# Kernel optimization log

Measured on AMD Instinct MI355X. Metric: run time of the kernel, lower is better.

The kernel has to match this reference:

```python
import jax, jax.numpy as jnp
import numpy as np

E = 300000
N_ATOMS = 10000
C = 256
RBF = 16
NUM_TARGET = 1


def setup_inputs() -> dict:
    key = jax.random.key(0)
    ks = jax.random.split(key, 12)
    s = lambda fan_in: 1.0 / np.sqrt(fan_in)
    return {
        "x": jax.random.normal(ks[0], (E, C), dtype=jnp.float32),
        "rbf": jax.random.uniform(ks[1], (E, RBF), dtype=jnp.float32),
        "num_atoms": N_ATOMS,
        "edge_index_0": jax.random.randint(ks[2], (E,), 0, N_ATOMS, dtype=jnp.int64),
        # lin_rbf: Linear(rbf_dim -> in_channels)
        "w_rbf": jax.random.normal(ks[3], (C, RBF), dtype=jnp.float32) * s(RBF),
        "b_rbf": jnp.zeros((C,), dtype=jnp.float32),
        # mlp: Linear(C,C), SiLU, Linear(C,C), SiLU, Linear(C, num_target)
        "w1": jax.random.normal(ks[4], (C, C), dtype=jnp.float32) * s(C),
        "b1": jnp.zeros((C,), dtype=jnp.float32),
        "w2": jax.random.normal(ks[5], (C, C), dtype=jnp.float32) * s(C),
        "b2": jnp.zeros((C,), dtype=jnp.float32),
        "w3": jax.random.normal(ks[6], (NUM_TARGET, C), dtype=jnp.float32) * s(C),
        "b3": jnp.zeros((NUM_TARGET,), dtype=jnp.float32),
    }


def reference(x, rbf, num_atoms, edge_index_0, w_rbf, b_rbf, w1, b1, w2, b2, w3, b3):
    # rbf_filter = lin_rbf(rbf): [E, C]
    rbf_filter = rbf @ w_rbf.T + b_rbf
    msg = rbf_filter * x  # [E, C]
    # scatter_add over edge source -> per-atom features [num_atoms, C]
    out = jax.ops.segment_sum(msg, edge_index_0, num_segments=num_atoms)
    # MLP: Linear+SiLU, Linear+SiLU, Linear
    out = jax.nn.silu(out @ w1.T + b1)
    out = jax.nn.silu(out @ w2.T + b2)
    out = out @ w3.T + b3  # [num_atoms, num_target]
    return out
```

## Files before the change

### kernel.cpp

```cpp
#include <hip/hip_runtime.h>
#include <math.h>

#define CDIM 256
#define RBFD 16
#define NATOMS 10000

__device__ __forceinline__ float dot44(float4 a, float4 b) {
  return a.x * b.x + a.y * b.y + a.z * b.z + a.w * b.w;
}

__global__ void hist_kernel(const int* __restrict__ eidx, int* __restrict__ counts,
                            int E) {
  const int i = blockIdx.x * blockDim.x + threadIdx.x;
  if (i < E) atomicAdd(&counts[eidx[i]], 1);
}

__global__ void scan_kernel(const int* __restrict__ counts,
                            int* __restrict__ offsets, int* __restrict__ cursor) {
  __shared__ int part[256];
  const int t = threadIdx.x;
  const int CH = (NATOMS + 255) / 256;
  const int base = t * CH;
  const int n = min(CH, max(0, NATOMS - base));
  int s = 0;
  for (int j = 0; j < n; ++j) s += counts[base + j];
  part[t] = s;
  __syncthreads();
  for (int off = 1; off < 256; off <<= 1) {
    int v = 0;
    if (t >= off) v = part[t - off];
    __syncthreads();
    part[t] += v;
    __syncthreads();
  }
  int run = part[t] - s;
  for (int j = 0; j < n; ++j) {
    offsets[base + j] = run;
    cursor[base + j] = run;
    run += counts[base + j];
  }
  if (t == 255) offsets[NATOMS] = part[255];
}

__global__ void scatter_kernel(const int* __restrict__ eidx,
                               int* __restrict__ cursor, int* __restrict__ elist,
                               int E) {
  const int i = blockIdx.x * blockDim.x + threadIdx.x;
  if (i < E) {
    const int a = eidx[i];
    const int pos = atomicAdd(&cursor[a], 1);
    elist[pos] = i;
  }
}

__global__ __launch_bounds__(256, 5) void gather_kernel(
    const float* __restrict__ x, const float* __restrict__ rbf,
    const int* __restrict__ elist, const int* __restrict__ offsets,
    const float* __restrict__ w_rbf, const float* __restrict__ b_rbf,
    float* __restrict__ acc) {
  const int tid = threadIdx.x;
  const int lane = tid & 63;
  const int w = tid >> 6;
  const int atom = blockIdx.x;
  const int ch = w * 64 + lane;

  const int start = __builtin_amdgcn_readfirstlane(offsets[atom]);
  const int end = __builtin_amdgcn_readfirstlane(offsets[atom + 1]);

  float4 wv0, wv1, wv2, wv3;
  {
    const float4* wr = (const float4*)(w_rbf + (size_t)ch * RBFD);
    wv0 = wr[0];
    wv1 = wr[1];
    wv2 = wr[2];
    wv3 = wr[3];
  }
  const float bb = b_rbf[ch];

  if (end <= start) {
    acc[(size_t)atom * CDIM + ch] = 0.f;
    return;
  }
  const int last = end - 1;

  float sumA = 0.f, sumB = 0.f, sumC = 0.f;

  float xA, xB, xC;
  float4 rA0, rA1, rA2, rA3;
  float4 rB0, rB1, rB2, rB3;
  float4 rC0, rC1, rC2, rC3;

#define LOADD(S, eid)                                                        \
  {                                                                          \
    x##S = x[(size_t)(eid)*CDIM + ch];           \
    const float4* q_ = (const float4*)(rbf + (size_t)(eid)*RBFD);            \
    r##S##0 = q_[0];                                                         \
    r##S##1 = q_[1];                                                         \
    r##S##2 = q_[2];                                                         \
    r##S##3 = q_[3];                                                         \
  }

#define COMPUTE(S, sum)                                                      \
  {                                                                          \
    const float f_ = bb + dot44(wv0, r##S##0) + dot44(wv1, r##S##1) +        \
                     dot44(wv2, r##S##2) + dot44(wv3, r##S##3);              \
    sum += f_ * x##S;                                                        \
  }

  int idA = __builtin_amdgcn_readfirstlane(elist[start]);
  int idB = __builtin_amdgcn_readfirstlane(elist[min(start + 1, last)]);
  int idC = __builtin_amdgcn_readfirstlane(elist[min(start + 2, last)]);
  LOADD(A, idA)
  LOADD(B, idB)

  int i = start;
  for (; i + 3 <= end; i += 3) {
    idA = __builtin_amdgcn_readfirstlane(elist[min(i + 3, last)]);
    LOADD(C, idC)
    COMPUTE(A, sumA)
    idB = __builtin_amdgcn_readfirstlane(elist[min(i + 4, last)]);
    LOADD(A, idA)
    COMPUTE(B, sumB)
    idC = __builtin_amdgcn_readfirstlane(elist[min(i + 5, last)]);
    LOADD(B, idB)
    COMPUTE(C, sumC)
  }
  const int k = end - i;
  if (k >= 1) COMPUTE(A, sumA)
  if (k >= 2) COMPUTE(B, sumB)

#undef LOADD
#undef COMPUTE

  acc[(size_t)atom * CDIM + ch] = sumA + sumB + sumC;
}

__global__ void transpose_kernel(const float* __restrict__ w1,
                                 const float* __restrict__ w2,
                                 float* __restrict__ w1T,
                                 float* __restrict__ w2T) {
  __shared__ float tile[32][33];
  const float* src = blockIdx.z ? w2 : w1;
  float* dst = blockIdx.z ? w2T : w1T;
  const int bx = blockIdx.x * 32;
  const int by = blockIdx.y * 32;
  const int tx = threadIdx.x, ty = threadIdx.y;
#pragma unroll
  for (int i = 0; i < 32; i += 8)
    tile[ty + i][tx] = src[(size_t)(by + ty + i) * CDIM + bx + tx];
  __syncthreads();
#pragma unroll
  for (int i = 0; i < 32; i += 8)
    dst[(size_t)(bx + ty + i) * CDIM + by + tx] = tile[tx][ty + i];
}

__global__ __launch_bounds__(256, 2) void mlp_kernel(
    const float* __restrict__ hin, const float* __restrict__ w1T,
    const float* __restrict__ b1, const float* __restrict__ w2T,
    const float* __restrict__ b2, const float* __restrict__ w3,
    const float* __restrict__ b3, float* __restrict__ out, int natoms) {
  __shared__ float H[32 * 256];
  __shared__ float WK[32 * 256];
  const int tid = threadIdx.x;
  const int tc = tid & 31;
  const int ta = tid >> 5;
  const int a0 = blockIdx.x * 32;
  const int cA = tc * 4;
  const int cB = 128 + tc * 4;

  {
    const float4* src = (const float4*)hin + (size_t)a0 * 64;
    float4* Hv = (float4*)H;
#pragma unroll
    for (int i = 0; i < 8; ++i) {
      const int idx = tid + i * 256;
      const int ga = a0 + (idx >> 6);
      Hv[idx] = (ga < natoms) ? src[idx] : make_float4(0.f, 0.f, 0.f, 0.f);
    }
  }

  float s[4][8];

#pragma unroll 1
  for (int layer = 0; layer < 2; ++layer) {
    const float* wT = (layer == 0) ? w1T : w2T;
    const float* bias = (layer == 0) ? b1 : b2;
    float r[4][8];
    const float4 bA = *(const float4*)(bias + cA);
    const float4 bB = *(const float4*)(bias + cB);
#pragma unroll
    for (int a = 0; a < 4; ++a) {
      r[a][0] = bA.x; r[a][1] = bA.y; r[a][2] = bA.z; r[a][3] = bA.w;
      r[a][4] = bB.x; r[a][5] = bB.y; r[a][6] = bB.z; r[a][7] = bB.w;
    }

    for (int k0 = 0; k0 < 256; k0 += 32) {
      __syncthreads();
      {
        const float4* wsrc = (const float4*)(wT + (size_t)k0 * CDIM);
        float4* WKv = (float4*)WK;
#pragma unroll
        for (int i = 0; i < 8; ++i) WKv[tid + i * 256] = wsrc[tid + i * 256];
      }
      __syncthreads();

#pragma unroll
      for (int kk = 0; kk < 32; kk += 4) {
        float4 ha[4];
#pragma unroll
        for (int a = 0; a < 4; ++a)
          ha[a] = *(const float4*)&H[(ta * 4 + a) * 256 + k0 + kk];
#pragma unroll
        for (int u = 0; u < 4; ++u) {
          const float4 w0 = *(const float4*)&WK[(kk + u) * 256 + cA];
          const float4 w1v = *(const float4*)&WK[(kk + u) * 256 + cB];
#pragma unroll
          for (int a = 0; a < 4; ++a) {
            const float hv = (u == 0) ? ha[a].x
                           : (u == 1) ? ha[a].y
                           : (u == 2) ? ha[a].z : ha[a].w;
            r[a][0] += hv * w0.x;  r[a][1] += hv * w0.y;
            r[a][2] += hv * w0.z;  r[a][3] += hv * w0.w;
            r[a][4] += hv * w1v.x; r[a][5] += hv * w1v.y;
            r[a][6] += hv * w1v.z; r[a][7] += hv * w1v.w;
          }
        }
      }
    }

#pragma unroll
    for (int a = 0; a < 4; ++a)
#pragma unroll
      for (int j = 0; j < 8; ++j) {
        const float v = r[a][j];
        s[a][j] = v / (1.0f + __expf(-v));
      }

    if (layer == 0) {
      __syncthreads();
#pragma unroll
      for (int a = 0; a < 4; ++a) {
        *(float4*)&H[(ta * 4 + a) * 256 + cA] =
            make_float4(s[a][0], s[a][1], s[a][2], s[a][3]);
        *(float4*)&H[(ta * 4 + a) * 256 + cB] =
            make_float4(s[a][4], s[a][5], s[a][6], s[a][7]);
      }
    }
  }

  const float4 w3a = *(const float4*)(w3 + cA);
  const float4 w3b = *(const float4*)(w3 + cB);
  float part[4];
#pragma unroll
  for (int a = 0; a < 4; ++a) {
    part[a] = s[a][0] * w3a.x + s[a][1] * w3a.y + s[a][2] * w3a.z +
              s[a][3] * w3a.w + s[a][4] * w3b.x + s[a][5] * w3b.y +
              s[a][6] * w3b.z + s[a][7] * w3b.w;
  }
  __syncthreads();
  float* red = WK;
#pragma unroll
  for (int a = 0; a < 4; ++a) red[(ta * 4 + a) * 33 + tc] = part[a];
  __syncthreads();
  if (tid < 32) {
    float sum = 0.f;
#pragma unroll
    for (int j = 0; j < 32; ++j) sum += red[tid * 33 + j];
    const int ga = a0 + tid;
    if (ga < natoms) out[ga] = sum + b3[0];
  }
}

extern "C" void kernel_launch(void* const* d_in, const int* in_sizes, int n_in,
                              void* d_out, int out_size, void* d_ws,
                              size_t ws_size, hipStream_t stream) {
  const float* x = (const float*)d_in[0];
  const float* rbf = (const float*)d_in[1];
  const int* eidx = (const int*)d_in[3];
  const float* w_rbf = (const float*)d_in[4];
  const float* b_rbf = (const float*)d_in[5];
  const float* w1 = (const float*)d_in[6];
  const float* b1 = (const float*)d_in[7];
  const float* w2 = (const float*)d_in[8];
  const float* b2 = (const float*)d_in[9];
  const float* w3 = (const float*)d_in[10];
  const float* b3 = (const float*)d_in[11];
  float* out = (float*)d_out;
  const int E = in_sizes[0] / CDIM;

  char* p = (char*)d_ws;
  float* acc = (float*)p;              p += (size_t)NATOMS * CDIM * sizeof(float);
  float* w1T = (float*)p;              p += CDIM * CDIM * sizeof(float);
  float* w2T = (float*)p;              p += CDIM * CDIM * sizeof(float);
  int* counts = (int*)p;               p += NATOMS * sizeof(int);
  int* offsets = (int*)p;              p += (NATOMS + 1) * sizeof(int);
  int* cursor = (int*)p;               p += NATOMS * sizeof(int);
  int* elist = (int*)p;                p += (size_t)E * sizeof(int);

  hipMemsetAsync(counts, 0, NATOMS * sizeof(int), stream);
  hist_kernel<<<(E + 255) / 256, 256, 0, stream>>>(eidx, counts, E);
  scan_kernel<<<1, 256, 0, stream>>>(counts, offsets, cursor);
  scatter_kernel<<<(E + 255) / 256, 256, 0, stream>>>(eidx, cursor, elist, E);
  transpose_kernel<<<dim3(8, 8, 2), dim3(32, 8), 0, stream>>>(w1, w2, w1T, w2T);
  gather_kernel<<<NATOMS, 256, 0, stream>>>(x, rbf, elist, offsets, w_rbf,
                                            b_rbf, acc);
  mlp_kernel<<<(NATOMS + 31) / 32, 256, 0, stream>>>(acc, w1T, b1, w2T, b2, w3,
                                                     b3, out, NATOMS);
}
```

Baseline: 627.1 us.

## Deepen gather pipeline to 8-edge double-buffered batches of x loads

Restructures the per-atom gather loop so that x values for eight edges are loaded ahead in a double-buffered batch while the rbf filter values for the next batch are computed, and edge indices are prefetched two batches ahead. This is meant to keep more independent memory loads in flight and hide gather latency on the irregular x reads. Occupancy is lowered from 5 to 4 waves per SIMD via launch bounds to allow the larger register footprint. It adds wasted loads and compute for tail edges on atoms with few edges (about 30 edges per atom on average).

```diff
diff --git a/kernel.cpp b/kernel.cpp
--- a/kernel.cpp
+++ b/kernel.cpp
@@ -53,7 +53,7 @@
   }
 }
 
-__global__ __launch_bounds__(256, 5) void gather_kernel(
+__global__ __launch_bounds__(256, 4) void gather_kernel(
     const float* __restrict__ x, const float* __restrict__ rbf,
     const int* __restrict__ elist, const int* __restrict__ offsets,
     const float* __restrict__ w_rbf, const float* __restrict__ b_rbf,
@@ -83,56 +83,90 @@
   }
   const int last = end - 1;
 
-  float sumA = 0.f, sumB = 0.f, sumC = 0.f;
-
-  float xA, xB, xC;
-  float4 rA0, rA1, rA2, rA3;
-  float4 rB0, rB1, rB2, rB3;
-  float4 rC0, rC1, rC2, rC3;
-
-#define LOADD(S, eid)                                                        \
+  float sumE = 0.f, sumO = 0.f;
+  float xA[8], xB[8], fA[8], fB[8];
+  int idn[8];
+
+#define LOADX(XS)                                                            \
+  _Pragma("unroll") for (int j = 0; j < 8; ++j) {                            \
+    XS[j] = x[(size_t)idn[j] * CDIM + ch];                                   \
+  }
+
+#define LDR(Q, e)                                                            \
   {                                                                          \
-    x##S = x[(size_t)(eid)*CDIM + ch];           \
-    const float4* q_ = (const float4*)(rbf + (size_t)(eid)*RBFD);            \
-    r##S##0 = q_[0];                                                         \
-    r##S##1 = q_[1];                                                         \
-    r##S##2 = q_[2];                                                         \
-    r##S##3 = q_[3];                                                         \
-  }
-
-#define COMPUTE(S, sum)                                                      \
+    const float4* q_ = (const float4*)(rbf + (size_t)(e)*RBFD);              \
+    Q##0 = q_[0];                                                            \
+    Q##1 = q_[1];                                                            \
+    Q##2 = q_[2];                                                            \
+    Q##3 = q_[3];                                                            \
+  }
+
+#define FVAL(Q)                                                              \
+  (bb + dot44(wv0, Q##0) + dot44(wv1, Q##1) + dot44(wv2, Q##2) +             \
+   dot44(wv3, Q##3))
+
+#define PIPEF(FS)                                                            \
   {                                                                          \
-    const float f_ = bb + dot44(wv0, r##S##0) + dot44(wv1, r##S##1) +        \
-                     dot44(wv2, r##S##2) + dot44(wv3, r##S##3);              \
-    sum += f_ * x##S;                                                        \
-  }
-
-  int idA = __builtin_amdgcn_readfirstlane(elist[start]);
-  int idB = __builtin_amdgcn_readfirstlane(elist[min(start + 1, last)]);
-  int idC = __builtin_amdgcn_readfirstlane(elist[min(start + 2, last)]);
-  LOADD(A, idA)
-  LOADD(B, idB)
+    float4 p0, p1, p2, p3, q0, q1, q2, q3, r0, r1, r2, r3;                   \
+    LDR(p, idn[0]) LDR(q, idn[1]) LDR(r, idn[2])                             \
+    FS[0] = FVAL(p);                                                         \
+    LDR(p, idn[3])                                                           \
+    FS[1] = FVAL(q);                                                         \
+    LDR(q, idn[4])                                                           \
+    FS[2] = FVAL(r);                                                         \
+    LDR(r, idn[5])                                                           \
+    FS[3] = FVAL(p);                                                         \
+    LDR(p, idn[6])                                                           \
+    FS[4] = FVAL(q);                                                         \
+    LDR(q, idn[7])                                                           \
+    FS[5] = FVAL(r);                                                         \
+    FS[6] = FVAL(p);                                                         \
+    FS[7] = FVAL(q);                                                         \
+  }
+
+#define CONSUME(XS, FS, i0)                                                  \
+  _Pragma("unroll") for (int j = 0; j < 8; ++j) {                            \
+    if ((i0) + j < end) {                                                    \
+      if (j & 1) sumO += FS[j] * XS[j];                                      \
+      else sumE += FS[j] * XS[j];                                            \
+    }                                                                        \
+  }
+
+#define REFILL(i0)                                                           \
+  _Pragma("unroll") for (int j = 0; j < 8; ++j) {                            \
+    idn[j] = __builtin_amdgcn_readfirstlane(elist[min((i0) + j, last)]);     \
+  }
+
+#define PHASE(XC, FC, XN, FN, i0)                                            \
+  LOADX(XN)                                                                  \
+  PIPEF(FN)                                                                  \
+  CONSUME(XC, FC, i0)                                                        \
+  REFILL((i0) + 16)
+
+  REFILL(start)
+  LOADX(xA)
+  PIPEF(fA)
+  REFILL(start + 8)
 
   int i = start;
-  for (; i + 3 <= end; i += 3) {
-    idA = __builtin_amdgcn_readfirstlane(elist[min(i + 3, last)]);
-    LOADD(C, idC)
-    COMPUTE(A, sumA)
-    idB = __builtin_amdgcn_readfirstlane(elist[min(i + 4, last)]);
-    LOADD(A, idA)
-    COMPUTE(B, sumB)
-    idC = __builtin_amdgcn_readfirstlane(elist[min(i + 5, last)]);
-    LOADD(B, idB)
-    COMPUTE(C, sumC)
-  }
-  const int k = end - i;
-  if (k >= 1) COMPUTE(A, sumA)
-  if (k >= 2) COMPUTE(B, sumB)
-
-#undef LOADD
-#undef COMPUTE
-
-  acc[(size_t)atom * CDIM + ch] = sumA + sumB + sumC;
+  while (true) {
+    PHASE(xA, fA, xB, fB, i)
+    i += 8;
+    if (i >= end) break;
+    PHASE(xB, fB, xA, fA, i)
+    i += 8;
+    if (i >= end) break;
+  }
+
+#undef LOADX
+#undef LDR
+#undef FVAL
+#undef PIPEF
+#undef CONSUME
+#undef REFILL
+#undef PHASE
+
+  acc[(size_t)atom * CDIM + ch] = sumE + sumO;
 }
 
 __global__ void transpose_kernel(const float* __restrict__ w1,
```

Measured after the change: 642.2 us. +2.4%, slower.
